# Performance work log

Measured on AMD Instinct MI355X. Metric: run time of the kernel, lower is better.

Reference implementation:

```python
import jax, jax.numpy as jnp
import numpy as np

M = 8        # number of input features
NMF = 4      # membership functions per feature
R = NMF ** M # 65536 rules
N = 1024     # batch size


def setup_inputs() -> dict:
    key = jax.random.key(0)
    k1, k2, k3, k4, k5 = jax.random.split(key, 5)
    x = jax.random.normal(k1, (N, M), dtype=jnp.float32)
    # Antecedent parameters: torch.rand -> uniform [0,1)
    center = jax.random.uniform(k2, (M, NMF), dtype=jnp.float32)
    sigma = jax.random.uniform(k3, (M, NMF), dtype=jnp.float32)
    # Consequent linear layer, init_Consequent uses uniform [0,1)
    W = jax.random.uniform(k4, (R, M), dtype=jnp.float32)
    b = jax.random.uniform(k5, (R,), dtype=jnp.float32)
    return {"x": x, "center": center, "sigma": sigma, "W": W, "b": b}


def reference(x, center, sigma, W, b):
    # droprule=False (deterministic reference; the torch drop_rule is random Bernoulli masking)
    n = x.shape[0]
    # Gaussian membership, faithful to torch: exp(-(x - c)^2 / 2 * sigma^2)
    # mg: [N, M, NMF]
    mg = jnp.exp(-((x[:, :, None] - center[None, :, :]) ** 2) * 0.5 * (sigma[None, :, :] ** 2))
    # Combinatorial rule product via mixed-radix broadcasting:
    # fg[n, r] = prod_m mg[n, m, digit_m(r)], feature 0 most significant.
    fg = mg[:, 0, :]  # [N, NMF]
    for m in range(1, M):
        fg = (fg[:, :, None] * mg[:, m, None, :]).reshape(n, -1)
    # fg: [N, R]
    fg_bar = fg / jnp.sum(fg, axis=1, keepdims=True)
    rule_out = x @ W.T + b  # [N, R]
    return jnp.sum(fg_bar * rule_out, axis=1)  # [N]
```

## Files before the change

kernel.cpp:

```cpp
#include <hip/hip_runtime.h>
#include <hip/hip_bf16.h>

typedef __attribute__((ext_vector_type(8))) short short8;
typedef __attribute__((ext_vector_type(4))) float f32x4;

#define KB 16

__device__ __forceinline__ ushort f2bf(float f) {
    __hip_bfloat16 h = __float2bfloat16(f);
    return *reinterpret_cast<ushort*>(&h);
}
__device__ __forceinline__ unsigned pk2(float a, float b) {
    return (unsigned)f2bf(a) | ((unsigned)f2bf(b) << 16);
}

__global__ __launch_bounds__(256) void fz_main(
    const float* __restrict__ x, const float* __restrict__ center,
    const float* __restrict__ sigma, const float* __restrict__ W,
    const float* __restrict__ b, float* __restrict__ out, int N)
{
    __shared__ float  mgs[16][33];
    __shared__ float  pr[16][20]  __attribute__((aligned(16)));
    __shared__ float  phs[KB][20] __attribute__((aligned(16)));
    __shared__ float  red[4][16][9];
    __shared__ ushort wstg[4][2][8][17][8] __attribute__((aligned(16)));

    const int t = threadIdx.x;
    const int tile = blockIdx.x >> 4;
    const int kb = blockIdx.x & (KB - 1);

    #pragma unroll
    for (int v = 0; v < 2; ++v) {
        int id = t + v * 256;
        int s = id >> 5, i = id & 31, m = i >> 2;
        float xv = x[(size_t)(tile * 16 + s) * 8 + m];
        float d = xv - center[i];
        float sg = sigma[i];
        mgs[s][i] = __expf(-d * d * 0.5f * sg * sg);
    }
    __syncthreads();
    {
        int s = t >> 4, a = t & 15;
        pr[s][a] = mgs[s][24 + (a >> 2)] * mgs[s][28 + (a & 3)];
    }
    {
        int hil = t >> 4, s = t & 15;
        int hi = kb * KB + hil;
        phs[hil][s] = mgs[s][hi >> 6] * mgs[s][4 + ((hi >> 4) & 3)]
                    * mgs[s][8 + ((hi >> 2) & 3)] * mgs[s][12 + (hi & 3)];
    }
    __syncthreads();

    const int wv = t >> 6, lane = t & 63;
    const int c = lane & 15, kb4 = lane >> 4;

    short8 A[2];
    {
        const int s_a = lane & 15;
        #pragma unroll
        for (int q = 0; q < 2; ++q) {
            const int ls = 2 * wv + q;
            const int L0 = ls * 32 + kb4 * 8;
            const float pq = mgs[s_a][16 + (L0 >> 6)] * mgs[s_a][20 + ((L0 >> 4) & 3)];
            const int b7 = L0 & 8;
            const float4 r0 = *reinterpret_cast<const float4*>(&pr[s_a][b7]);
            const float4 r1 = *reinterpret_cast<const float4*>(&pr[s_a][b7 + 4]);
            unsigned Pk[4] = { pk2(pq * r0.x, pq * r0.y), pk2(pq * r0.z, pq * r0.w),
                               pk2(pq * r1.x, pq * r1.y), pk2(pq * r1.z, pq * r1.w) };
            A[q] = *reinterpret_cast<short8*>(&Pk[0]);
        }
    }

    const float*  wrow = W + ((size_t)kb * 4096 + 64 * wv + lane) * 8;
    const float*  brow = b + kb * 4096 + 64 * wv + lane;
    ushort* rg = &wstg[wv][0][0][0][0];

    auto sload = [&](int hil, float4& wa, float4& wb, float& bv) {
        wa = *reinterpret_cast<const float4*>(wrow + hil * 2048);
        wb = *reinterpret_cast<const float4*>(wrow + hil * 2048 + 4);
        bv = brow[hil * 256];
    };
    auto swrite = [&](int buf, const float4& wa, const float4& wb, float bv) {
        ushort* p = rg + buf * 1088 + (lane >> 3) * 136 + (lane & 7);
        p[0]  = f2bf(wa.x); p[8]  = f2bf(wa.y); p[16] = f2bf(wa.z); p[24] = f2bf(wa.w);
        p[32] = f2bf(wb.x); p[40] = f2bf(wb.y); p[48] = f2bf(wb.z); p[56] = f2bf(wb.w);
        p[64] = f2bf(bv);
    };

    float4 wa, wb2; float bv;
    sload(0, wa, wb2, bv);
    swrite(0, wa, wb2, bv);

    f32x4 master = {0.f, 0.f, 0.f, 0.f};
    #pragma unroll 4
    for (int hil = 0; hil < KB; ++hil) {
        const int buf = hil & 1;
        if (hil + 1 < KB) sload(hil + 1, wa, wb2, bv);
        const ushort* q = rg + buf * 1088 + kb4 * 136 + c * 8;
        short8 B0 = *reinterpret_cast<const short8*>(q);
        short8 B1 = *reinterpret_cast<const short8*>(q + 4 * 136);
        f32x4 d = {0.f, 0.f, 0.f, 0.f};
        d = __builtin_amdgcn_mfma_f32_16x16x32_bf16(A[0], B0, d, 0, 0, 0);
        d = __builtin_amdgcn_mfma_f32_16x16x32_bf16(A[1], B1, d, 0, 0, 0);
        const float4 phv = *reinterpret_cast<const float4*>(&phs[hil][kb4 * 4]);
        master[0] += phv.x * d[0]; master[1] += phv.y * d[1];
        master[2] += phv.z * d[2]; master[3] += phv.w * d[3];
        if (hil + 1 < KB) swrite(buf ^ 1, wa, wb2, bv);
    }

    if (c < 9) {
        #pragma unroll
        for (int r = 0; r < 4; ++r)
            red[wv][kb4 * 4 + r][c] = master[r];
    }
    __syncthreads();
    if (t < 144) {
        int s = t / 9, cc = t % 9;
        red[0][s][cc] += red[1][s][cc] + red[2][s][cc] + red[3][s][cc];
    }
    __syncthreads();
    if (t < 16) {
        const int s = t;
        float denom = 1.f;
        #pragma unroll
        for (int m = 0; m < 8; ++m)
            denom *= (mgs[s][4 * m] + mgs[s][4 * m + 1] +
                      mgs[s][4 * m + 2] + mgs[s][4 * m + 3]);
        float num = red[0][s][8];
        #pragma unroll
        for (int m = 0; m < 8; ++m)
            num += x[(size_t)(tile * 16 + s) * 8 + m] * red[0][s][m];
        atomicAdd(&out[tile * 16 + s], num / denom);
    }
}

extern "C" void kernel_launch(void* const* d_in, const int* in_sizes, int n_in,
                              void* d_out, int out_size, void* d_ws, size_t ws_size,
                              hipStream_t stream)
{
    const float* x      = (const float*)d_in[0];
    const float* center = (const float*)d_in[1];
    const float* sigma  = (const float*)d_in[2];
    const float* W      = (const float*)d_in[3];
    const float* b      = (const float*)d_in[4];
    float* out = (float*)d_out;
    const int N = in_sizes[0] / 8;

    hipMemsetAsync(out, 0, (size_t)out_size * sizeof(float), stream);
    fz_main<<<(N / 16) * KB, 256, 0, stream>>>(x, center, sigma, W, b, out, N);
}
```

Baseline: 71.00 us.

## Process 32 samples per block to reuse each staged W tile twice

Each block now handles 32 samples (two 16-row MFMA tiles) instead of 16, and the rule range per block shrinks from 16 to 8 high-digit groups, with KB doubled to 32. Every W/b chunk loaded and converted to bf16 therefore feeds two sample tiles. This halves the total global W traffic and conversion work across the grid while keeping the grid size at 1024 blocks. The cost is more registers for the extra A fragments and accumulators, and a shorter per-block loop that exposes more prologue overhead.

```diff
diff --git a/kernel.cpp b/kernel.cpp
--- a/kernel.cpp
+++ b/kernel.cpp
@@ -4,7 +4,9 @@
 typedef __attribute__((ext_vector_type(8))) short short8;
 typedef __attribute__((ext_vector_type(4))) float f32x4;
 
-#define KB 16
+#define KB 32
+#define HPB 8
+#define SPT 32
 
 __device__ __forceinline__ ushort f2bf(float f) {
     __hip_bfloat16 h = __float2bfloat16(f);
@@ -19,33 +21,34 @@
     const float* __restrict__ sigma, const float* __restrict__ W,
     const float* __restrict__ b, float* __restrict__ out, int N)
 {
-    __shared__ float  mgs[16][33];
-    __shared__ float  pr[16][20]  __attribute__((aligned(16)));
-    __shared__ float  phs[KB][20] __attribute__((aligned(16)));
-    __shared__ float  red[4][16][9];
+    __shared__ float  mgs[SPT][33];
+    __shared__ float  pr[SPT][20]  __attribute__((aligned(16)));
+    __shared__ float  phs[HPB][36] __attribute__((aligned(16)));
+    __shared__ float  red[4][SPT][9];
     __shared__ ushort wstg[4][2][8][17][8] __attribute__((aligned(16)));
 
     const int t = threadIdx.x;
-    const int tile = blockIdx.x >> 4;
+    const int tile = blockIdx.x >> 5;
     const int kb = blockIdx.x & (KB - 1);
 
     #pragma unroll
-    for (int v = 0; v < 2; ++v) {
+    for (int v = 0; v < 4; ++v) {
         int id = t + v * 256;
         int s = id >> 5, i = id & 31, m = i >> 2;
-        float xv = x[(size_t)(tile * 16 + s) * 8 + m];
+        float xv = x[(size_t)(tile * SPT + s) * 8 + m];
         float d = xv - center[i];
         float sg = sigma[i];
         mgs[s][i] = __expf(-d * d * 0.5f * sg * sg);
     }
     __syncthreads();
-    {
-        int s = t >> 4, a = t & 15;
+    #pragma unroll
+    for (int v = 0; v < 2; ++v) {
+        int s = (t >> 4) + v * 16, a = t & 15;
         pr[s][a] = mgs[s][24 + (a >> 2)] * mgs[s][28 + (a & 3)];
     }
     {
-        int hil = t >> 4, s = t & 15;
-        int hi = kb * KB + hil;
+        int hil = t >> 5, s = t & 31;
+        int hi = kb * HPB + hil;
         phs[hil][s] = mgs[s][hi >> 6] * mgs[s][4 + ((hi >> 4) & 3)]
                     * mgs[s][8 + ((hi >> 2) & 3)] * mgs[s][12 + (hi & 3)];
     }
@@ -54,9 +57,10 @@
     const int wv = t >> 6, lane = t & 63;
     const int c = lane & 15, kb4 = lane >> 4;
 
-    short8 A[2];
-    {
-        const int s_a = lane & 15;
+    short8 A[2][2];
+    #pragma unroll
+    for (int st = 0; st < 2; ++st) {
+        const int s_a = st * 16 + (lane & 15);
         #pragma unroll
         for (int q = 0; q < 2; ++q) {
             const int ls = 2 * wv + q;
@@ -67,12 +71,12 @@
             const float4 r1 = *reinterpret_cast<const float4*>(&pr[s_a][b7 + 4]);
             unsigned Pk[4] = { pk2(pq * r0.x, pq * r0.y), pk2(pq * r0.z, pq * r0.w),
                                pk2(pq * r1.x, pq * r1.y), pk2(pq * r1.z, pq * r1.w) };
-            A[q] = *reinterpret_cast<short8*>(&Pk[0]);
+            A[st][q] = *reinterpret_cast<short8*>(&Pk[0]);
         }
     }
 
-    const float*  wrow = W + ((size_t)kb * 4096 + 64 * wv + lane) * 8;
-    const float*  brow = b + kb * 4096 + 64 * wv + lane;
+    const float* wrow = W + ((size_t)kb * 2048 + 64 * wv + lane) * 8;
+    const float* brow = b + kb * 2048 + 64 * wv + lane;
     ushort* rg = &wstg[wv][0][0][0][0];
 
     auto sload = [&](int hil, float4& wa, float4& wb, float& bv) {
@@ -91,35 +95,41 @@
     sload(0, wa, wb2, bv);
     swrite(0, wa, wb2, bv);
 
-    f32x4 master = {0.f, 0.f, 0.f, 0.f};
+    f32x4 master[2] = {{0.f, 0.f, 0.f, 0.f}, {0.f, 0.f, 0.f, 0.f}};
     #pragma unroll 4
-    for (int hil = 0; hil < KB; ++hil) {
+    for (int hil = 0; hil < HPB; ++hil) {
         const int buf = hil & 1;
-        if (hil + 1 < KB) sload(hil + 1, wa, wb2, bv);
+        if (hil + 1 < HPB) sload(hil + 1, wa, wb2, bv);
         const ushort* q = rg + buf * 1088 + kb4 * 136 + c * 8;
         short8 B0 = *reinterpret_cast<const short8*>(q);
         short8 B1 = *reinterpret_cast<const short8*>(q + 4 * 136);
-        f32x4 d = {0.f, 0.f, 0.f, 0.f};
-        d = __builtin_amdgcn_mfma_f32_16x16x32_bf16(A[0], B0, d, 0, 0, 0);
-        d = __builtin_amdgcn_mfma_f32_16x16x32_bf16(A[1], B1, d, 0, 0, 0);
-        const float4 phv = *reinterpret_cast<const float4*>(&phs[hil][kb4 * 4]);
-        master[0] += phv.x * d[0]; master[1] += phv.y * d[1];
-        master[2] += phv.z * d[2]; master[3] += phv.w * d[3];
-        if (hil + 1 < KB) swrite(buf ^ 1, wa, wb2, bv);
+        #pragma unroll
+        for (int st = 0; st < 2; ++st) {
+            f32x4 d = {0.f, 0.f, 0.f, 0.f};
+            d = __builtin_amdgcn_mfma_f32_16x16x32_bf16(A[st][0], B0, d, 0, 0, 0);
+            d = __builtin_amdgcn_mfma_f32_16x16x32_bf16(A[st][1], B1, d, 0, 0, 0);
+            const float4 phv =
+                *reinterpret_cast<const float4*>(&phs[hil][st * 16 + kb4 * 4]);
+            master[st][0] += phv.x * d[0]; master[st][1] += phv.y * d[1];
+            master[st][2] += phv.z * d[2]; master[st][3] += phv.w * d[3];
+        }
+        if (hil + 1 < HPB) swrite(buf ^ 1, wa, wb2, bv);
     }
 
     if (c < 9) {
         #pragma unroll
-        for (int r = 0; r < 4; ++r)
-            red[wv][kb4 * 4 + r][c] = master[r];
+        for (int st = 0; st < 2; ++st)
+            #pragma unroll
+            for (int r = 0; r < 4; ++r)
+                red[wv][st * 16 + kb4 * 4 + r][c] = master[st][r];
     }
     __syncthreads();
-    if (t < 144) {
-        int s = t / 9, cc = t % 9;
+    for (int id = t; id < SPT * 9; id += 256) {
+        int s = id / 9, cc = id % 9;
         red[0][s][cc] += red[1][s][cc] + red[2][s][cc] + red[3][s][cc];
     }
     __syncthreads();
-    if (t < 16) {
+    if (t < SPT) {
         const int s = t;
         float denom = 1.f;
         #pragma unroll
@@ -129,8 +139,8 @@
         float num = red[0][s][8];
         #pragma unroll
         for (int m = 0; m < 8; ++m)
-            num += x[(size_t)(tile * 16 + s) * 8 + m] * red[0][s][m];
-        atomicAdd(&out[tile * 16 + s], num / denom);
+            num += x[(size_t)(tile * SPT + s) * 8 + m] * red[0][s][m];
+        atomicAdd(&out[tile * SPT + s], num / denom);
     }
 }
 
@@ -147,5 +157,5 @@
     const int N = in_sizes[0] / 8;
 
     hipMemsetAsync(out, 0, (size_t)out_size * sizeof(float), stream);
-    fz_main<<<(N / 16) * KB, 256, 0, stream>>>(x, center, sigma, W, b, out, N);
+    fz_main<<<(N / SPT) * KB, 256, 0, stream>>>(x, center, sigma, W, b, out, N);
 }
```

New measurement: 69.91 us. About the same (-1.5%).
